# Kernel optimization log

Hardware: AMD Instinct MI355X
Metric: run time of the kernel (lower is better)

## Reference

```python
import jax, jax.numpy as jnp
import numpy as np

D, HID, P, BS = 256, 64, 2, 1024


def _xavier(key, shape):
    # xavier_uniform with leaky_relu gain ~= sqrt(2/(1+0.01^2))
    fan_out, fan_in = shape[-2], shape[-1]
    gain = float(np.sqrt(2.0 / (1.0 + 0.01 ** 2)))
    bound = gain * float(np.sqrt(6.0 / (fan_in + fan_out)))
    return jax.random.uniform(key, shape, jnp.float32, -bound, bound)


def setup_inputs() -> dict:
    key = jax.random.key(0)
    ks = jax.random.split(key, 8)
    x = jax.random.normal(ks[0], (BS, D), jnp.float32)
    # Stochastic Gumbel-sigmoid mask sample, one (d,d) mask per batch element
    M = jax.random.uniform(ks[1], (BS, D, D), jnp.float32)
    adj = jnp.ones((D, D), jnp.float32) - jnp.eye(D, dtype=jnp.float32)
    W0 = _xavier(ks[2], (D, HID, D))   # per-node first layer: (t, i, j)
    b0 = jnp.zeros((D, HID), jnp.float32)
    W1 = _xavier(ks[3], (D, HID, HID))
    b1 = jnp.zeros((D, HID), jnp.float32)
    W2 = _xavier(ks[4], (D, P, HID))
    b2 = jnp.zeros((D, P), jnp.float32)
    return {"x": x, "M": M, "adj": adj, "W0": W0, "b0": b0,
            "W1": W1, "b1": b1, "W2": W2, "b2": b2}


def reference(x, M, adj, W0, b0, W1, b1, W2, b2):
    # Layer 0: einsum('tij,bjt,ljt,bj->bti', W0, M, adj, x) + b0
    # Fuse the three elementwise factors first: (b, j, t)
    xmask = M * adj[None, :, :] * x[:, :, None]
    h = jnp.einsum('tij,bjt->bti', W0, xmask) + b0          # (b, d, hid)
    h = jax.nn.leaky_relu(h)
    # Hidden layer: einsum('tij,btj->bti')
    h = jnp.einsum('tij,btj->bti', W1, h) + b1              # (b, d, hid)
    h = jax.nn.leaky_relu(h)
    # Output layer
    out = jnp.einsum('tij,btj->bti', W2, h) + b2            # (b, d, num_params)
    # torch returns torch.unbind(out, 1); we return the stacked equivalent
    return out
```

## Files before the change

kernel.cpp:

```cpp
#include <hip/hip_runtime.h>
#include <cstdint>

#define Dd   256
#define HID  64
#define Pp   2
#define BSz  1024
#define BB   16
#define TT   16
#define JC   8
#define NT   512
#define WSTR 68
#define XSTR 20

__global__ __launch_bounds__(NT, 4)
void fused_mlp_v2(const float* __restrict__ x,
                  const float* __restrict__ M,
                  const float* __restrict__ W0,
                  const float* __restrict__ b0,
                  const float* __restrict__ W1,
                  const float* __restrict__ b1,
                  const float* __restrict__ W2,
                  const float* __restrict__ b2,
                  float* __restrict__ out)
{
    __shared__ float ws[JC * TT * WSTR];
    __shared__ float xm[JC * TT * XSTR];

    const int tid = threadIdx.x;

    const int ig = tid & 7;
    const int bg = (tid >> 3) & 3;
    const int tc = tid >> 5;
    const int t4 = tid & 3;
    const int bs = (tid >> 2) & 15;
    const int jg = tid >> 6;
    const int jq = tid & 1;
    const int iw = (tid >> 1) & 63;
    const int tw = tid >> 7;

    const int orig = blockIdx.x;
    const int wgid = (orig & 7) * 128 + (orig >> 3);
    const int b0r  = (wgid & 63) * BB;
    const int t0   = (wgid >> 6) * TT;

    const float* Mp = M + (size_t)(b0r + bs) * (Dd * Dd) + t0 + t4 * 4;
    const float* xp = x + (size_t)(b0r + bs) * Dd;

    float acc[32];
#pragma unroll
    for (int k = 0; k < 32; ++k) acc[k] = 0.0f;

#pragma unroll 1
    for (int jc = 0; jc < Dd / JC; ++jc) {
        const int j0 = jc * JC;
        const float4 mv = *reinterpret_cast<const float4*>(Mp + (size_t)(j0 + jg) * Dd);
        const float  xv = xp[j0 + jg];
        float4 wv[4];
#pragma unroll
        for (int s = 0; s < 4; ++s) {
            const int t = s * 4 + tw;
            wv[s] = *reinterpret_cast<const float4*>(
                W0 + ((size_t)(t0 + t) * HID + iw) * Dd + j0 + jq * 4);
        }

        __syncthreads();

        {
            const int jglob = j0 + jg;
            const int tb = t0 + t4 * 4;
            float* dst = xm + (jg * TT + t4 * 4) * XSTR + bs;
            dst[0 * XSTR] = (jglob == tb + 0) ? 0.0f : mv.x * xv;
            dst[1 * XSTR] = (jglob == tb + 1) ? 0.0f : mv.y * xv;
            dst[2 * XSTR] = (jglob == tb + 2) ? 0.0f : mv.z * xv;
            dst[3 * XSTR] = (jglob == tb + 3) ? 0.0f : mv.w * xv;
        }
#pragma unroll
        for (int s = 0; s < 4; ++s) {
            const int t = s * 4 + tw;
            float* dst = ws + ((jq * 4) * TT + t) * WSTR + iw;
            dst[0 * TT * WSTR] = wv[s].x;
            dst[1 * TT * WSTR] = wv[s].y;
            dst[2 * TT * WSTR] = wv[s].z;
            dst[3 * TT * WSTR] = wv[s].w;
        }
        __syncthreads();

        const float* wsrow = ws + tc * WSTR + ig * 8;
        const float* xmrow = xm + tc * XSTR + bg * 4;
#pragma unroll
        for (int jj = 0; jj < JC; ++jj) {
            const float4 a  = *reinterpret_cast<const float4*>(xmrow + jj * TT * XSTR);
            const float4 wA = *reinterpret_cast<const float4*>(wsrow + jj * TT * WSTR);
            const float4 wB = *reinterpret_cast<const float4*>(wsrow + jj * TT * WSTR + 4);
            const float av[4]  = {a.x, a.y, a.z, a.w};
            const float wvv[8] = {wA.x, wA.y, wA.z, wA.w, wB.x, wB.y, wB.z, wB.w};
#pragma unroll
            for (int rb = 0; rb < 4; ++rb)
#pragma unroll
                for (int ii = 0; ii < 8; ++ii)
                    acc[rb * 8 + ii] = fmaf(av[rb], wvv[ii], acc[rb * 8 + ii]);
        }
    }

    float h[4][8];
    {
        const float4 ba = *reinterpret_cast<const float4*>(b0 + (size_t)(t0 + tc) * HID + ig * 8);
        const float4 bb = *reinterpret_cast<const float4*>(b0 + (size_t)(t0 + tc) * HID + ig * 8 + 4);
        const float bv[8] = {ba.x, ba.y, ba.z, ba.w, bb.x, bb.y, bb.z, bb.w};
#pragma unroll
        for (int rb = 0; rb < 4; ++rb)
#pragma unroll
            for (int ii = 0; ii < 8; ++ii) {
                const float v = acc[rb * 8 + ii] + bv[ii];
                h[rb][ii] = (v >= 0.0f) ? v : 0.01f * v;
            }
    }

    float acc2[32];
#pragma unroll
    for (int k = 0; k < 32; ++k) acc2[k] = 0.0f;

    const int laneBase = tid & 56;

#pragma unroll 1
    for (int jc = 0; jc < HID / JC; ++jc) {
        float4 wv[4];
#pragma unroll
        for (int s = 0; s < 4; ++s) {
            const int t = s * 4 + tw;
            wv[s] = *reinterpret_cast<const float4*>(
                W1 + ((size_t)(t0 + t) * HID + iw) * HID + jc * JC + jq * 4);
        }
        __syncthreads();
#pragma unroll
        for (int s = 0; s < 4; ++s) {
            const int t = s * 4 + tw;
            float* dst = ws + ((jq * 4) * TT + t) * WSTR + iw;
            dst[0 * TT * WSTR] = wv[s].x;
            dst[1 * TT * WSTR] = wv[s].y;
            dst[2 * TT * WSTR] = wv[s].z;
            dst[3 * TT * WSTR] = wv[s].w;
        }
        __syncthreads();

        const float* wsrow = ws + tc * WSTR + ig * 8;
#pragma unroll
        for (int jj = 0; jj < JC; ++jj) {
            const float4 wA = *reinterpret_cast<const float4*>(wsrow + jj * TT * WSTR);
            const float4 wB = *reinterpret_cast<const float4*>(wsrow + jj * TT * WSTR + 4);
            const float wvv[8] = {wA.x, wA.y, wA.z, wA.w, wB.x, wB.y, wB.z, wB.w};
            const float h0 = __shfl(h[0][jj], laneBase + jc, 64);
            const float h1 = __shfl(h[1][jj], laneBase + jc, 64);
            const float h2 = __shfl(h[2][jj], laneBase + jc, 64);
            const float h3 = __shfl(h[3][jj], laneBase + jc, 64);
            const float hv[4] = {h0, h1, h2, h3};
#pragma unroll
            for (int rb = 0; rb < 4; ++rb)
#pragma unroll
                for (int ii = 0; ii < 8; ++ii)
                    acc2[rb * 8 + ii] = fmaf(hv[rb], wvv[ii], acc2[rb * 8 + ii]);
        }
    }

    float h2[4][8];
    {
        const float4 ba = *reinterpret_cast<const float4*>(b1 + (size_t)(t0 + tc) * HID + ig * 8);
        const float4 bb = *reinterpret_cast<const float4*>(b1 + (size_t)(t0 + tc) * HID + ig * 8 + 4);
        const float bv[8] = {ba.x, ba.y, ba.z, ba.w, bb.x, bb.y, bb.z, bb.w};
#pragma unroll
        for (int rb = 0; rb < 4; ++rb)
#pragma unroll
            for (int ii = 0; ii < 8; ++ii) {
                const float v = acc2[rb * 8 + ii] + bv[ii];
                h2[rb][ii] = (v >= 0.0f) ? v : 0.01f * v;
            }
    }

    const float* w2p = W2 + (size_t)(t0 + tc) * Pp * HID + ig * 8;
    const float4 wa0 = *reinterpret_cast<const float4*>(w2p);
    const float4 wa1 = *reinterpret_cast<const float4*>(w2p + 4);
    const float4 wb0 = *reinterpret_cast<const float4*>(w2p + HID);
    const float4 wb1 = *reinterpret_cast<const float4*>(w2p + HID + 4);
    const float w2v0[8] = {wa0.x, wa0.y, wa0.z, wa0.w, wa1.x, wa1.y, wa1.z, wa1.w};
    const float w2v1[8] = {wb0.x, wb0.y, wb0.z, wb0.w, wb1.x, wb1.y, wb1.z, wb1.w};

    float po[4][2];
#pragma unroll
    for (int rb = 0; rb < 4; ++rb) { po[rb][0] = 0.0f; po[rb][1] = 0.0f; }
#pragma unroll
    for (int rb = 0; rb < 4; ++rb)
#pragma unroll
        for (int jj = 0; jj < 8; ++jj) {
            po[rb][0] = fmaf(w2v0[jj], h2[rb][jj], po[rb][0]);
            po[rb][1] = fmaf(w2v1[jj], h2[rb][jj], po[rb][1]);
        }
#pragma unroll
    for (int d = 1; d < 8; d <<= 1)
#pragma unroll
        for (int rb = 0; rb < 4; ++rb) {
            po[rb][0] += __shfl_xor(po[rb][0], d, 64);
            po[rb][1] += __shfl_xor(po[rb][1], d, 64);
        }

    if (ig == 0) {
        const float2 b2v = *reinterpret_cast<const float2*>(b2 + (size_t)(t0 + tc) * Pp);
#pragma unroll
        for (int rb = 0; rb < 4; ++rb) {
            float2 o;
            o.x = po[rb][0] + b2v.x;
            o.y = po[rb][1] + b2v.y;
            *reinterpret_cast<float2*>(
                out + ((size_t)(b0r + bg * 4 + rb) * Dd + (t0 + tc)) * Pp) = o;
        }
    }
}

extern "C" void kernel_launch(void* const* d_in, const int* in_sizes, int n_in,
                              void* d_out, int out_size, void* d_ws, size_t ws_size,
                              hipStream_t stream)
{
    const float* x  = (const float*)d_in[0];
    const float* M  = (const float*)d_in[1];
    const float* W0 = (const float*)d_in[3];
    const float* b0 = (const float*)d_in[4];
    const float* W1 = (const float*)d_in[5];
    const float* b1 = (const float*)d_in[6];
    const float* W2 = (const float*)d_in[7];
    const float* b2 = (const float*)d_in[8];
    float* out = (float*)d_out;

    const int grid = (BSz / BB) * (Dd / TT);
    fused_mlp_v2<<<grid, NT, 0, stream>>>(x, M, W0, b0, W1, b1, W2, b2, out);
}
```

Measured before the change: 615.6 us.

## Rewrite fused MLP with split-bf16 MFMA matrix cores and prefetched mask tiles

Replaces the scalar FMA inner products of the first two layers with 16x16x32 bf16 MFMA instructions. Each fp32 operand is split into high and low bf16 parts, and three MFMAs per tile approximate fp32 accuracy. Weights are loaded straight from global memory into registers instead of being staged through LDS. The mask/x tile is software-prefetched one chunk ahead and the third layer is fused into the second layer's epilogue. This trades extra conversion arithmetic and possible precision loss for matrix-core throughput, but the kernel may still be bound by the bandwidth of streaming M.

Result: faster. 578.8 us (-6.0%).

```diff
diff --git a/kernel.cpp b/kernel.cpp
--- a/kernel.cpp
+++ b/kernel.cpp
@@ -1,4 +1,5 @@
 #include <hip/hip_runtime.h>
+#include <hip/hip_bf16.h>
 #include <cstdint>
 
 #define Dd   256
@@ -7,210 +8,214 @@
 #define BSz  1024
 #define BB   16
 #define TT   16
-#define JC   8
 #define NT   512
-#define WSTR 68
-#define XSTR 20
+#define XMS  36
+#define HBS  68
+
+typedef __attribute__((ext_vector_type(8))) short bf16x8;
+typedef __attribute__((ext_vector_type(4))) float f32x4;
+
+__device__ __forceinline__ short f2bf(float f) {
+    return __builtin_bit_cast(short, __float2bfloat16(f));
+}
+__device__ __forceinline__ float bf2f(short s) {
+    return __bfloat162float(__builtin_bit_cast(__hip_bfloat16, s));
+}
+
+__device__ __forceinline__ void split8(const float a[8], bf16x8& hi, bf16x8& lo) {
+#pragma unroll
+    for (int e = 0; e < 8; ++e) {
+        const short h = f2bf(a[e]);
+        hi[e] = h;
+        lo[e] = f2bf(a[e] - bf2f(h));
+    }
+}
 
 __global__ __launch_bounds__(NT, 4)
-void fused_mlp_v2(const float* __restrict__ x,
-                  const float* __restrict__ M,
-                  const float* __restrict__ W0,
-                  const float* __restrict__ b0,
-                  const float* __restrict__ W1,
-                  const float* __restrict__ b1,
-                  const float* __restrict__ W2,
-                  const float* __restrict__ b2,
+void fused_mlp_v3(const float* __restrict__ x,  const float* __restrict__ M,
+                  const float* __restrict__ W0, const float* __restrict__ b0,
+                  const float* __restrict__ W1, const float* __restrict__ b1,
+                  const float* __restrict__ W2, const float* __restrict__ b2,
                   float* __restrict__ out)
 {
-    __shared__ float ws[JC * TT * WSTR];
-    __shared__ float xm[JC * TT * XSTR];
-
-    const int tid = threadIdx.x;
-
-    const int ig = tid & 7;
-    const int bg = (tid >> 3) & 3;
-    const int tc = tid >> 5;
-    const int t4 = tid & 3;
-    const int bs = (tid >> 2) & 15;
-    const int jg = tid >> 6;
-    const int jq = tid & 1;
-    const int iw = (tid >> 1) & 63;
-    const int tw = tid >> 7;
+    __shared__ float smem[TT * BB * XMS];
+
+    const int tid  = threadIdx.x;
+    const int lane = tid & 63;
+    const int w    = tid >> 6;
+    const int ln15 = lane & 15;
+    const int lg   = lane >> 4;
 
     const int orig = blockIdx.x;
     const int wgid = (orig & 7) * 128 + (orig >> 3);
     const int b0r  = (wgid & 63) * BB;
     const int t0   = (wgid >> 6) * TT;
 
-    const float* Mp = M + (size_t)(b0r + bs) * (Dd * Dd) + t0 + t4 * 4;
-    const float* xp = x + (size_t)(b0r + bs) * Dd;
-
-    float acc[32];
-#pragma unroll
-    for (int k = 0; k < 32; ++k) acc[k] = 0.0f;
+    const int jloc = tid & 31;
+    const int bst  = tid >> 5;
+    const float* Mp = M + ((size_t)(b0r + bst) * Dd) * Dd + t0;
+    const float* xp = x + (size_t)(b0r + bst) * Dd;
+
+    f32x4 acc[2][4];
+#pragma unroll
+    for (int a = 0; a < 2; ++a)
+#pragma unroll
+        for (int b = 0; b < 4; ++b)
+            acc[a][b] = f32x4{0.f, 0.f, 0.f, 0.f};
+
+    float4 m0, m1, m2, m3; float xv;
+    {
+        const float* mp = Mp + (size_t)jloc * Dd;
+        m0 = *(const float4*)(mp + 0);  m1 = *(const float4*)(mp + 4);
+        m2 = *(const float4*)(mp + 8);  m3 = *(const float4*)(mp + 12);
+        xv = xp[jloc];
+    }
 
 #pragma unroll 1
-    for (int jc = 0; jc < Dd / JC; ++jc) {
-        const int j0 = jc * JC;
-        const float4 mv = *reinterpret_cast<const float4*>(Mp + (size_t)(j0 + jg) * Dd);
-        const float  xv = xp[j0 + jg];
-        float4 wv[4];
-#pragma unroll
-        for (int s = 0; s < 4; ++s) {
-            const int t = s * 4 + tw;
-            wv[s] = *reinterpret_cast<const float4*>(
-                W0 + ((size_t)(t0 + t) * HID + iw) * Dd + j0 + jq * 4);
-        }
-
-        __syncthreads();
-
+    for (int kc = 0; kc < 8; ++kc) {
+        __syncthreads();
+
+        const int kn = (kc < 7) ? kc + 1 : 7;
+        float4 n0, n1, n2, n3; float xn;
         {
-            const int jglob = j0 + jg;
-            const int tb = t0 + t4 * 4;
-            float* dst = xm + (jg * TT + t4 * 4) * XSTR + bs;
-            dst[0 * XSTR] = (jglob == tb + 0) ? 0.0f : mv.x * xv;
-            dst[1 * XSTR] = (jglob == tb + 1) ? 0.0f : mv.y * xv;
-            dst[2 * XSTR] = (jglob == tb + 2) ? 0.0f : mv.z * xv;
-            dst[3 * XSTR] = (jglob == tb + 3) ? 0.0f : mv.w * xv;
-        }
-#pragma unroll
-        for (int s = 0; s < 4; ++s) {
-            const int t = s * 4 + tw;
-            float* dst = ws + ((jq * 4) * TT + t) * WSTR + iw;
-            dst[0 * TT * WSTR] = wv[s].x;
-            dst[1 * TT * WSTR] = wv[s].y;
-            dst[2 * TT * WSTR] = wv[s].z;
-            dst[3 * TT * WSTR] = wv[s].w;
-        }
-        __syncthreads();
-
-        const float* wsrow = ws + tc * WSTR + ig * 8;
-        const float* xmrow = xm + tc * XSTR + bg * 4;
-#pragma unroll
-        for (int jj = 0; jj < JC; ++jj) {
-            const float4 a  = *reinterpret_cast<const float4*>(xmrow + jj * TT * XSTR);
-            const float4 wA = *reinterpret_cast<const float4*>(wsrow + jj * TT * WSTR);
-            const float4 wB = *reinterpret_cast<const float4*>(wsrow + jj * TT * WSTR + 4);
-            const float av[4]  = {a.x, a.y, a.z, a.w};
-            const float wvv[8] = {wA.x, wA.y, wA.z, wA.w, wB.x, wB.y, wB.z, wB.w};
-#pragma unroll
-            for (int rb = 0; rb < 4; ++rb)
-#pragma unroll
-                for (int ii = 0; ii < 8; ++ii)
-                    acc[rb * 8 + ii] = fmaf(av[rb], wvv[ii], acc[rb * 8 + ii]);
-        }
-    }
-
-    float h[4][8];
-    {
-        const float4 ba = *reinterpret_cast<const float4*>(b0 + (size_t)(t0 + tc) * HID + ig * 8);
-        const float4 bb = *reinterpret_cast<const float4*>(b0 + (size_t)(t0 + tc) * HID + ig * 8 + 4);
-        const float bv[8] = {ba.x, ba.y, ba.z, ba.w, bb.x, bb.y, bb.z, bb.w};
-#pragma unroll
-        for (int rb = 0; rb < 4; ++rb)
-#pragma unroll
-            for (int ii = 0; ii < 8; ++ii) {
-                const float v = acc[rb * 8 + ii] + bv[ii];
-                h[rb][ii] = (v >= 0.0f) ? v : 0.01f * v;
-            }
-    }
-
-    float acc2[32];
-#pragma unroll
-    for (int k = 0; k < 32; ++k) acc2[k] = 0.0f;
-
-    const int laneBase = tid & 56;
+            const float* mp = Mp + (size_t)(kn * 32 + jloc) * Dd;
+            n0 = *(const float4*)(mp + 0);  n1 = *(const float4*)(mp + 4);
+            n2 = *(const float4*)(mp + 8);  n3 = *(const float4*)(mp + 12);
+            xn = xp[kn * 32 + jloc];
+        }
+
+        {
+            const int jg = kc * 32 + jloc;
+            float* xrow = smem + bst * XMS + jloc;
+            const float mv[16] = {m0.x, m0.y, m0.z, m0.w, m1.x, m1.y, m1.z, m1.w,
+                                  m2.x, m2.y, m2.z, m2.w, m3.x, m3.y, m3.z, m3.w};
+#pragma unroll
+            for (int tt = 0; tt < 16; ++tt) {
+                float v = mv[tt] * xv;
+                v = (jg == t0 + tt) ? 0.0f : v;
+                xrow[(size_t)tt * BB * XMS] = v;
+            }
+        }
+        __syncthreads();
+
+#pragma unroll
+        for (int tp = 0; tp < 2; ++tp) {
+            const int tloc = 2 * w + tp;
+            float af[8];
+            const float* ap = smem + ((size_t)(tloc * BB + ln15)) * XMS + lg * 8;
+            *(float4*)&af[0] = *(const float4*)ap;
+            *(float4*)&af[4] = *(const float4*)(ap + 4);
+            bf16x8 ahi, alo; split8(af, ahi, alo);
+
+            const float* wrow = W0 + (size_t)(t0 + tloc) * HID * Dd + kc * 32 + lg * 8;
+#pragma unroll
+            for (int it = 0; it < 4; ++it) {
+                float bf[8];
+                const float* bp = wrow + (size_t)(it * 16 + ln15) * Dd;
+                *(float4*)&bf[0] = *(const float4*)bp;
+                *(float4*)&bf[4] = *(const float4*)(bp + 4);
+                bf16x8 bhi, blo; split8(bf, bhi, blo);
+                acc[tp][it] = __builtin_amdgcn_mfma_f32_16x16x32_bf16(ahi, bhi, acc[tp][it], 0, 0, 0);
+                acc[tp][it] = __builtin_amdgcn_mfma_f32_16x16x32_bf16(ahi, blo, acc[tp][it], 0, 0, 0);
+                acc[tp][it] = __builtin_amdgcn_mfma_f32_16x16x32_bf16(alo, bhi, acc[tp][it], 0, 0, 0);
+            }
+        }
+        m0 = n0; m1 = n1; m2 = n2; m3 = n3; xv = xn;
+    }
+
+    float hreg[2][4][4];
+#pragma unroll
+    for (int tp = 0; tp < 2; ++tp) {
+        const int t = t0 + 2 * w + tp;
+#pragma unroll
+        for (int it = 0; it < 4; ++it) {
+            const float bv = b0[(size_t)t * HID + it * 16 + ln15];
+#pragma unroll
+            for (int r = 0; r < 4; ++r) {
+                const float v = acc[tp][it][r] + bv;
+                hreg[tp][it][r] = (v >= 0.f) ? v : 0.01f * v;
+            }
+        }
+    }
 
 #pragma unroll 1
-    for (int jc = 0; jc < HID / JC; ++jc) {
-        float4 wv[4];
-#pragma unroll
-        for (int s = 0; s < 4; ++s) {
-            const int t = s * 4 + tw;
-            wv[s] = *reinterpret_cast<const float4*>(
-                W1 + ((size_t)(t0 + t) * HID + iw) * HID + jc * JC + jq * 4);
-        }
-        __syncthreads();
-#pragma unroll
-        for (int s = 0; s < 4; ++s) {
-            const int t = s * 4 + tw;
-            float* dst = ws + ((jq * 4) * TT + t) * WSTR + iw;
-            dst[0 * TT * WSTR] = wv[s].x;
-            dst[1 * TT * WSTR] = wv[s].y;
-            dst[2 * TT * WSTR] = wv[s].z;
-            dst[3 * TT * WSTR] = wv[s].w;
-        }
-        __syncthreads();
-
-        const float* wsrow = ws + tc * WSTR + ig * 8;
-#pragma unroll
-        for (int jj = 0; jj < JC; ++jj) {
-            const float4 wA = *reinterpret_cast<const float4*>(wsrow + jj * TT * WSTR);
-            const float4 wB = *reinterpret_cast<const float4*>(wsrow + jj * TT * WSTR + 4);
-            const float wvv[8] = {wA.x, wA.y, wA.z, wA.w, wB.x, wB.y, wB.z, wB.w};
-            const float h0 = __shfl(h[0][jj], laneBase + jc, 64);
-            const float h1 = __shfl(h[1][jj], laneBase + jc, 64);
-            const float h2 = __shfl(h[2][jj], laneBase + jc, 64);
-            const float h3 = __shfl(h[3][jj], laneBase + jc, 64);
-            const float hv[4] = {h0, h1, h2, h3};
-#pragma unroll
-            for (int rb = 0; rb < 4; ++rb)
-#pragma unroll
-                for (int ii = 0; ii < 8; ++ii)
-                    acc2[rb * 8 + ii] = fmaf(hv[rb], wvv[ii], acc2[rb * 8 + ii]);
-        }
-    }
-
-    float h2[4][8];
-    {
-        const float4 ba = *reinterpret_cast<const float4*>(b1 + (size_t)(t0 + tc) * HID + ig * 8);
-        const float4 bb = *reinterpret_cast<const float4*>(b1 + (size_t)(t0 + tc) * HID + ig * 8 + 4);
-        const float bv[8] = {ba.x, ba.y, ba.z, ba.w, bb.x, bb.y, bb.z, bb.w};
-#pragma unroll
-        for (int rb = 0; rb < 4; ++rb)
-#pragma unroll
-            for (int ii = 0; ii < 8; ++ii) {
-                const float v = acc2[rb * 8 + ii] + bv[ii];
-                h2[rb][ii] = (v >= 0.0f) ? v : 0.01f * v;
-            }
-    }
-
-    const float* w2p = W2 + (size_t)(t0 + tc) * Pp * HID + ig * 8;
-    const float4 wa0 = *reinterpret_cast<const float4*>(w2p);
-    const float4 wa1 = *reinterpret_cast<const float4*>(w2p + 4);
-    const float4 wb0 = *reinterpret_cast<const float4*>(w2p + HID);
-    const float4 wb1 = *reinterpret_cast<const float4*>(w2p + HID + 4);
-    const float w2v0[8] = {wa0.x, wa0.y, wa0.z, wa0.w, wa1.x, wa1.y, wa1.z, wa1.w};
-    const float w2v1[8] = {wb0.x, wb0.y, wb0.z, wb0.w, wb1.x, wb1.y, wb1.z, wb1.w};
-
-    float po[4][2];
-#pragma unroll
-    for (int rb = 0; rb < 4; ++rb) { po[rb][0] = 0.0f; po[rb][1] = 0.0f; }
-#pragma unroll
-    for (int rb = 0; rb < 4; ++rb)
-#pragma unroll
-        for (int jj = 0; jj < 8; ++jj) {
-            po[rb][0] = fmaf(w2v0[jj], h2[rb][jj], po[rb][0]);
-            po[rb][1] = fmaf(w2v1[jj], h2[rb][jj], po[rb][1]);
-        }
-#pragma unroll
-    for (int d = 1; d < 8; d <<= 1)
-#pragma unroll
-        for (int rb = 0; rb < 4; ++rb) {
-            po[rb][0] += __shfl_xor(po[rb][0], d, 64);
-            po[rb][1] += __shfl_xor(po[rb][1], d, 64);
-        }
-
-    if (ig == 0) {
-        const float2 b2v = *reinterpret_cast<const float2*>(b2 + (size_t)(t0 + tc) * Pp);
-#pragma unroll
-        for (int rb = 0; rb < 4; ++rb) {
-            float2 o;
-            o.x = po[rb][0] + b2v.x;
-            o.y = po[rb][1] + b2v.y;
-            *reinterpret_cast<float2*>(
-                out + ((size_t)(b0r + bg * 4 + rb) * Dd + (t0 + tc)) * Pp) = o;
+    for (int pass = 0; pass < 2; ++pass) {
+        __syncthreads();
+
+        if ((w >> 2) == pass) {
+            const int wl = w & 3;
+#pragma unroll
+            for (int tp = 0; tp < 2; ++tp) {
+                const int tlp = 2 * wl + tp;
+#pragma unroll
+                for (int it = 0; it < 4; ++it)
+#pragma unroll
+                    for (int r = 0; r < 4; ++r)
+                        smem[(size_t)(tlp * BB + lg * 4 + r) * HBS + it * 16 + ln15] =
+                            hreg[tp][it][r];
+            }
+        }
+        __syncthreads();
+
+        const int t = t0 + pass * 8 + w;
+        f32x4 acc2[4];
+#pragma unroll
+        for (int it = 0; it < 4; ++it) acc2[it] = f32x4{0.f, 0.f, 0.f, 0.f};
+
+#pragma unroll
+        for (int kc2 = 0; kc2 < 2; ++kc2) {
+            float af[8];
+            const float* ap = smem + (size_t)(w * BB + ln15) * HBS + kc2 * 32 + lg * 8;
+            *(float4*)&af[0] = *(const float4*)ap;
+            *(float4*)&af[4] = *(const float4*)(ap + 4);
+            bf16x8 ahi, alo; split8(af, ahi, alo);
+
+            const float* w1row = W1 + (size_t)t * HID * HID + kc2 * 32 + lg * 8;
+#pragma unroll
+            for (int it = 0; it < 4; ++it) {
+                float bf[8];
+                const float* bp = w1row + (size_t)(it * 16 + ln15) * HID;
+                *(float4*)&bf[0] = *(const float4*)bp;
+                *(float4*)&bf[4] = *(const float4*)(bp + 4);
+                bf16x8 bhi, blo; split8(bf, bhi, blo);
+                acc2[it] = __builtin_amdgcn_mfma_f32_16x16x32_bf16(ahi, bhi, acc2[it], 0, 0, 0);
+                acc2[it] = __builtin_amdgcn_mfma_f32_16x16x32_bf16(ahi, blo, acc2[it], 0, 0, 0);
+                acc2[it] = __builtin_amdgcn_mfma_f32_16x16x32_bf16(alo, bhi, acc2[it], 0, 0, 0);
+            }
+        }
+
+        float po0[4] = {0.f, 0.f, 0.f, 0.f};
+        float po1[4] = {0.f, 0.f, 0.f, 0.f};
+#pragma unroll
+        for (int it = 0; it < 4; ++it) {
+            const float b1v = b1[(size_t)t * HID + it * 16 + ln15];
+            const float w2a = W2[(size_t)t * Pp * HID + 0 * HID + it * 16 + ln15];
+            const float w2b = W2[(size_t)t * Pp * HID + 1 * HID + it * 16 + ln15];
+#pragma unroll
+            for (int r = 0; r < 4; ++r) {
+                float v = acc2[it][r] + b1v;
+                v = (v >= 0.f) ? v : 0.01f * v;
+                po0[r] = fmaf(w2a, v, po0[r]);
+                po1[r] = fmaf(w2b, v, po1[r]);
+            }
+        }
+#pragma unroll
+        for (int d = 1; d < 16; d <<= 1)
+#pragma unroll
+            for (int r = 0; r < 4; ++r) {
+                po0[r] += __shfl_xor(po0[r], d, 64);
+                po1[r] += __shfl_xor(po1[r], d, 64);
+            }
+        if (ln15 == 0) {
+            const float2 b2v = *(const float2*)(b2 + (size_t)t * Pp);
+#pragma unroll
+            for (int r = 0; r < 4; ++r) {
+                const int bg = lg * 4 + r;
+                float2 o;
+                o.x = po0[r] + b2v.x;
+                o.y = po1[r] + b2v.y;
+                *(float2*)(out + ((size_t)(b0r + bg) * Dd + t) * Pp) = o;
+            }
         }
     }
 }
@@ -230,5 +235,5 @@
     float* out = (float*)d_out;
 
     const int grid = (BSz / BB) * (Dd / TT);
-    fused_mlp_v2<<<grid, NT, 0, stream>>>(x, M, W0, b0, W1, b1, W2, b2, out);
-}
+    fused_mlp_v3<<<grid, NT, 0, stream>>>(x, M, W0, b0, W1, b1, W2, b2, out);
+}
```
